# Kernel optimization log

Hardware: AMD Instinct MI355X
Metric: run time of the kernel (lower is better)

The kernel has to match this reference:

```python
import jax, jax.numpy as jnp
import numpy as np

EMBED_DIM = 1024
NUM_HEADS = 16
HEAD_DIM = EMBED_DIM // NUM_HEADS
B, S = 4, 2048


def setup_inputs() -> dict:
    key = jax.random.key(0)
    ks = jax.random.split(key, 9)
    scale = 1.0 / np.sqrt(EMBED_DIM)
    x = jax.random.normal(ks[0], (B, S, EMBED_DIM), dtype=jnp.float32)
    # nn.Linear weights are [out, in]; we store as [in, out] for x @ W
    Wq = jax.random.uniform(ks[1], (EMBED_DIM, EMBED_DIM), jnp.float32, -scale, scale)
    bq = jax.random.uniform(ks[2], (EMBED_DIM,), jnp.float32, -scale, scale)
    Wk = jax.random.uniform(ks[3], (EMBED_DIM, EMBED_DIM), jnp.float32, -scale, scale)
    bk = jax.random.uniform(ks[4], (EMBED_DIM,), jnp.float32, -scale, scale)
    Wv = jax.random.uniform(ks[5], (EMBED_DIM, EMBED_DIM), jnp.float32, -scale, scale)
    bv = jax.random.uniform(ks[6], (EMBED_DIM,), jnp.float32, -scale, scale)
    Wo = jax.random.uniform(ks[7], (EMBED_DIM, EMBED_DIM), jnp.float32, -scale, scale)
    bo = jax.random.uniform(ks[8], (EMBED_DIM,), jnp.float32, -scale, scale)
    return {"x": x, "Wq": Wq, "bq": bq, "Wk": Wk, "bk": bk,
            "Wv": Wv, "bv": bv, "Wo": Wo, "bo": bo}


def reference(x, Wq, bq, Wk, bk, Wv, bv, Wo, bo):
    Bsz, Slen, E = x.shape
    H, D = NUM_HEADS, HEAD_DIM
    # projections -> [B, H, S, D]
    def split_heads(t):
        return t.reshape(Bsz, Slen, H, D).transpose(0, 2, 1, 3)
    q = split_heads(x @ Wq + bq)
    k = split_heads(x @ Wk + bk)
    v = split_heads(x @ Wv + bv)
    # scores [B, H, S, S]
    scores = jnp.einsum('bhqd,bhkd->bhqk', q, k) / jnp.sqrt(jnp.float32(D))
    attn = jax.nn.softmax(scores, axis=-1)  # dropout p=0.0 -> identity
    out = jnp.einsum('bhqk,bhkd->bhqd', attn, v)  # [B, H, S, D]
    out = out.transpose(0, 2, 1, 3).reshape(Bsz, Slen, E)
    return out @ Wo + bo
```

## Files before the change

### kernel.cpp

```cpp
#include <hip/hip_runtime.h>

typedef __bf16 bf16x8 __attribute__((ext_vector_type(8)));
typedef float floatx4 __attribute__((ext_vector_type(4)));

#define B_   4
#define H_   16
#define S_   2048
#define D_   64
#define E_   1024
#define BS_  8192

#define QSCALE 0.18033688011112042f

__device__ __forceinline__ floatx4 mfma16(bf16x8 a, bf16x8 b, floatx4 c) {
  return __builtin_amdgcn_mfma_f32_16x16x32_bf16(a, b, c, 0, 0, 0);
}

__device__ __forceinline__ unsigned short f2bf(float f) {
  union { float f; unsigned int u; } a;
  a.f = f;
  unsigned int u = a.u;
  return (unsigned short)((u + 0x7fffu + ((u >> 16) & 1u)) >> 16);
}

__device__ __forceinline__ unsigned int pack2bf(float a, float b) {
  union { float f; unsigned int u; } ua, ub;
  ua.f = a; ub.f = b;
  return __builtin_amdgcn_perm(ub.u + 0x8000u, ua.u + 0x8000u, 0x07060302u);
}

__device__ __forceinline__ void async16(const unsigned short* g, unsigned short* l) {
  __builtin_amdgcn_global_load_lds(
      (const __attribute__((address_space(1))) unsigned int*)g,
      (__attribute__((address_space(3))) unsigned int*)l, 16, 0, 0);
}

__global__ __launch_bounds__(256) void transpose4(
    const float* __restrict__ W0, const float* __restrict__ W1,
    const float* __restrict__ W2, const float* __restrict__ W3,
    unsigned short* __restrict__ Wt) {
  __shared__ float tile[32][33];
  const float* src = blockIdx.z == 0 ? W0 : blockIdx.z == 1 ? W1
                   : blockIdx.z == 2 ? W2 : W3;
  unsigned short* dst = Wt + (size_t)blockIdx.z * E_ * E_;
  const int k0 = blockIdx.x * 32, n0 = blockIdx.y * 32;
  const int tx = threadIdx.x, ty = threadIdx.y;
#pragma unroll
  for (int i = 0; i < 32; i += 8)
    tile[ty + i][tx] = src[(size_t)(k0 + ty + i) * E_ + n0 + tx];
  __syncthreads();
#pragma unroll
  for (int i = 0; i < 32; i += 8)
    dst[(size_t)(n0 + ty + i) * E_ + k0 + tx] = f2bf(tile[tx][ty + i]);
}

__global__ __launch_bounds__(256) void cast_x(
    const float* __restrict__ x, unsigned short* __restrict__ xb) {
  const size_t i = ((size_t)blockIdx.x * 256 + threadIdx.x) * 8;
  const float4* p = (const float4*)(x + i);
  float4 a0 = p[0], a1 = p[1];
  union { unsigned short h[8]; uint4 u; } pk;
  pk.h[0] = f2bf(a0.x); pk.h[1] = f2bf(a0.y); pk.h[2] = f2bf(a0.z); pk.h[3] = f2bf(a0.w);
  pk.h[4] = f2bf(a1.x); pk.h[5] = f2bf(a1.y); pk.h[6] = f2bf(a1.z); pk.h[7] = f2bf(a1.w);
  *(uint4*)(xb + i) = pk.u;
}

#define GEMM_CORE(APTR, BPTR)                                                  \
  __shared__ __align__(16) unsigned short As[128][32];                         \
  __shared__ __align__(16) unsigned short Bs[128][32];                         \
  const int t = threadIdx.x;                                                   \
  const int w = t >> 6, lane = t & 63, quad = lane >> 4, l15 = lane & 15;      \
  const int moff = (w >> 1) * 64, noff = (w & 1) * 64;                         \
  const int m0 = blockIdx.y * 128, n0 = blockIdx.x * 128;                      \
  const int r_loc = lane >> 2, cphys = lane & 3;                               \
  const int r0 = w * 32 + r_loc, r1 = r0 + 16;                                 \
  const int sw = (r0 & 3) ^ ((r0 >> 2) & 1);         \
  const int clog = (cphys ^ sw) * 8;                                           \
  const unsigned short* gA0 = (APTR) + (size_t)(m0 + r0) * E_ + clog;          \
  const unsigned short* gA1 = (APTR) + (size_t)(m0 + r1) * E_ + clog;          \
  const unsigned short* gB0 = (BPTR) + (size_t)(n0 + r0) * E_ + clog;          \
  const unsigned short* gB1 = (BPTR) + (size_t)(n0 + r1) * E_ + clog;          \
  unsigned short* lA0 = &As[w * 32][0];                                        \
  unsigned short* lA1 = &As[w * 32 + 16][0];                                   \
  unsigned short* lB0 = &Bs[w * 32][0];                                        \
  unsigned short* lB1 = &Bs[w * 32 + 16][0];                                   \
  const int sF = (l15 & 3) ^ ((l15 >> 2) & 1);          \
  const int fcol = ((quad ^ sF)) * 8;                                          \
  floatx4 acc[4][4] = {};                                                      \
  for (int k0 = 0; k0 < E_; k0 += 32) {                                        \
    async16(gA0 + k0, lA0);                                                    \
    async16(gA1 + k0, lA1);                                                    \
    async16(gB0 + k0, lB0);                                                    \
    async16(gB1 + k0, lB1);                                                    \
    __syncthreads();                     \
    bf16x8 af[4], bf[4];                                                       \
    _Pragma("unroll")                                                          \
    for (int i = 0; i < 4; i++)                                                \
      af[i] = *(const bf16x8*)&As[moff + i * 16 + l15][fcol];                  \
    _Pragma("unroll")                                                          \
    for (int j = 0; j < 4; j++)                                                \
      bf[j] = *(const bf16x8*)&Bs[noff + j * 16 + l15][fcol];                  \
    _Pragma("unroll")                                                          \
    for (int i = 0; i < 4; i++)                                                \
      _Pragma("unroll")                                                        \
      for (int j = 0; j < 4; j++) acc[i][j] = mfma16(af[i], bf[j], acc[i][j]); \
    __syncthreads();                              \
  }

__global__ __launch_bounds__(256) void gemm_qkv(
    const unsigned short* __restrict__ xb, const unsigned short* __restrict__ Wt,
    const float* __restrict__ bq, const float* __restrict__ bk,
    const float* __restrict__ bv,
    unsigned short* __restrict__ Q, unsigned short* __restrict__ K,
    unsigned short* __restrict__ V) {
  GEMM_CORE(xb, Wt)

  const int which = n0 >> 10;
  const float* bias = which == 0 ? bq : (which == 1 ? bk : bv);
  unsigned short* dst = which == 0 ? Q : (which == 1 ? K : V);
  const float sc = which == 0 ? QSCALE : 1.0f;
#pragma unroll
  for (int j = 0; j < 4; j++) {
    const int n = (n0 + noff + j * 16 + l15) & 1023;
    const int h = n >> 6, d = n & 63;
    const float bb = bias[n];
#pragma unroll
    for (int i = 0; i < 4; i++) {
#pragma unroll
      for (int r = 0; r < 4; r++) {
        const int m = m0 + moff + i * 16 + quad * 4 + r;
        const int b = m >> 11, s = m & 2047;
        const float val = (acc[i][j][r] + bb) * sc;
        if (which == 2) {
          const int sp = (s & ~63) | (((s & 15) << 2) | ((s >> 4) & 3));
          dst[(((size_t)(b * H_ + h) * D_) + d) * S_ + sp] = f2bf(val);
        } else {
          dst[(((size_t)(b * H_ + h) * S_) + s) * D_ + d] = f2bf(val);
        }
      }
    }
  }
}

__global__ __launch_bounds__(256, 4) void attn_kernel(
    const unsigned short* __restrict__ Q, const unsigned short* __restrict__ K,
    const unsigned short* __restrict__ Vt, unsigned short* __restrict__ AO) {
  __shared__ __align__(16) unsigned short Ks[64][72];
  __shared__ __align__(16) unsigned short Vs[64][72];
  __shared__ __align__(16) unsigned short Ps[128][72];
  const int t = threadIdx.x;
  const int w = t >> 6, lane = t & 63, quad = lane >> 4, l15 = lane & 15;
  const int bh = blockIdx.y;
  const int q0 = blockIdx.x * 128;
  const int qb = w * 32;
  const size_t base = (size_t)bh * S_ * D_;

  bf16x8 qf[2][2];
#pragma unroll
  for (int mt = 0; mt < 2; mt++)
#pragma unroll
    for (int ks = 0; ks < 2; ks++)
      qf[mt][ks] = *(const bf16x8*)(Q + base +
                    (size_t)(q0 + qb + mt * 16 + l15) * D_ + ks * 32 + quad * 8);

  float l_i[2][4] = {};
  floatx4 O[2][4] = {};

  const int kk = t >> 2, cc = (t & 3) * 16;
  const unsigned short* kp = K  + base + (size_t)kk * D_ + cc;
  const unsigned short* vp = Vt + base + (size_t)kk * S_ + cc;

  uint4 kr0 = *(const uint4*)(kp);
  uint4 kr1 = *(const uint4*)(kp + 8);
  uint4 vr0 = *(const uint4*)(vp);
  uint4 vr1 = *(const uint4*)(vp + 8);

  for (int kt0 = 0; kt0 < S_; kt0 += 64) {
    *(uint4*)&Ks[kk][cc]     = kr0;
    *(uint4*)&Ks[kk][cc + 8] = kr1;
    *(uint4*)&Vs[kk][cc]     = vr0;
    *(uint4*)&Vs[kk][cc + 8] = vr1;
    __syncthreads();

    if (kt0 + 64 < S_) {
      kr0 = *(const uint4*)(kp + (size_t)(kt0 + 64) * D_);
      kr1 = *(const uint4*)(kp + (size_t)(kt0 + 64) * D_ + 8);
      vr0 = *(const uint4*)(vp + kt0 + 64);
      vr1 = *(const uint4*)(vp + kt0 + 72);
    }

    floatx4 s[2][4] = {};
#pragma unroll
    for (int kt = 0; kt < 4; kt++) {
#pragma unroll
      for (int ks = 0; ks < 2; ks++) {
        bf16x8 kf = *(const bf16x8*)&Ks[kt * 16 + l15][ks * 32 + quad * 8];
#pragma unroll
        for (int mt = 0; mt < 2; mt++) s[mt][kt] = mfma16(qf[mt][ks], kf, s[mt][kt]);
      }
    }

#pragma unroll
    for (int mt = 0; mt < 2; mt++) {
#pragma unroll
      for (int r = 0; r < 4; r++) {
        const float p0 = __builtin_amdgcn_exp2f(s[mt][0][r]);
        const float p1 = __builtin_amdgcn_exp2f(s[mt][1][r]);
        const float p2 = __builtin_amdgcn_exp2f(s[mt][2][r]);
        const float p3 = __builtin_amdgcn_exp2f(s[mt][3][r]);
        l_i[mt][r] += (p0 + p1) + (p2 + p3);
        uint2 pk;
        pk.x = pack2bf(p0, p1);
        pk.y = pack2bf(p2, p3);
        *(uint2*)((char*)&Ps[qb + mt * 16 + quad * 4 + r][0] + l15 * 8) = pk;
      }
    }

#pragma unroll
    for (int ks = 0; ks < 2; ks++) {
      bf16x8 pf[2];
#pragma unroll
      for (int mt = 0; mt < 2; mt++)
        pf[mt] = *(const bf16x8*)&Ps[qb + mt * 16 + l15][ks * 32 + quad * 8];
#pragma unroll
      for (int dt = 0; dt < 4; dt++) {
        bf16x8 vf = *(const bf16x8*)&Vs[dt * 16 + l15][ks * 32 + quad * 8];
#pragma unroll
        for (int mt = 0; mt < 2; mt++) O[mt][dt] = mfma16(pf[mt], vf, O[mt][dt]);
      }
    }
    __syncthreads();
  }

  const int b = bh >> 4, h = bh & 15;
#pragma unroll
  for (int mt = 0; mt < 2; mt++)
#pragma unroll
    for (int r = 0; r < 4; r++) {
      float sum = l_i[mt][r];
#pragma unroll
      for (int off = 1; off < 16; off <<= 1) sum += __shfl_xor(sum, off, 64);
      const float inv = 1.f / sum;
      const int srow = q0 + qb + mt * 16 + quad * 4 + r;
      unsigned short* aop = AO + (size_t)(b * S_ + srow) * E_ + h * D_ + l15;
#pragma unroll
      for (int dt = 0; dt < 4; dt++)
        aop[dt * 16] = f2bf(O[mt][dt][r] * inv);
    }
}

__global__ __launch_bounds__(256) void gemm_out(
    const unsigned short* __restrict__ A, const unsigned short* __restrict__ Wt,
    const float* __restrict__ bo, float* __restrict__ Cout) {
  GEMM_CORE(A, Wt)

#pragma unroll
  for (int j = 0; j < 4; j++) {
    const int n = n0 + noff + j * 16 + l15;
    const float bb = bo[n];
#pragma unroll
    for (int i = 0; i < 4; i++) {
#pragma unroll
      for (int r = 0; r < 4; r++) {
        const int m = m0 + moff + i * 16 + quad * 4 + r;
        Cout[(size_t)m * E_ + n] = acc[i][j][r] + bb;
      }
    }
  }
}

extern "C" void kernel_launch(void* const* d_in, const int* in_sizes, int n_in,
                              void* d_out, int out_size, void* d_ws, size_t ws_size,
                              hipStream_t stream) {
  const float* x  = (const float*)d_in[0];
  const float* Wq = (const float*)d_in[1];
  const float* bq = (const float*)d_in[2];
  const float* Wk = (const float*)d_in[3];
  const float* bk = (const float*)d_in[4];
  const float* Wv = (const float*)d_in[5];
  const float* bv = (const float*)d_in[6];
  const float* Wo = (const float*)d_in[7];
  const float* bo = (const float*)d_in[8];
  float* out = (float*)d_out;

  unsigned short* Wt = (unsigned short*)d_ws;
  unsigned short* Qb = Wt + (size_t)4 * E_ * E_;
  unsigned short* Kb = Qb + (size_t)B_ * H_ * S_ * D_;
  unsigned short* Vb = Kb + (size_t)B_ * H_ * S_ * D_;
  unsigned short* xb = Vb + (size_t)B_ * H_ * S_ * D_;
  unsigned short* AO = xb;

  transpose4<<<dim3(32, 32, 4), dim3(32, 8), 0, stream>>>(Wq, Wk, Wv, Wo, Wt);
  cast_x<<<dim3(BS_ * E_ / (256 * 8)), 256, 0, stream>>>(x, xb);
  gemm_qkv<<<dim3(24, 64), 256, 0, stream>>>(xb, Wt, bq, bk, bv, Qb, Kb, Vb);
  attn_kernel<<<dim3(16, 64), 256, 0, stream>>>(Qb, Kb, Vb, AO);
  gemm_out<<<dim3(8, 64), 256, 0, stream>>>(AO, Wt + (size_t)3 * E_ * E_, bo, out);
}
```

Before: 318.7 us.

## Triple-buffer GEMM LDS tiles and prefetch next K-slice during MFMA compute

The shared GEMM core now keeps three LDS buffers for the A and B tiles. Before computing on the current slice, it issues the async global-to-LDS loads for the next K slice, which cuts the loop to one barrier per iteration instead of two. The aim is to hide global load latency behind the MFMA work. The cost is three times the LDS footprint (about 48KB per block), which may lower occupancy, and correctness relies on the barrier waiting for the outstanding async loads.

```diff
diff --git a/kernel.cpp b/kernel.cpp
--- a/kernel.cpp
+++ b/kernel.cpp
@@ -66,8 +66,8 @@
 }
 
 #define GEMM_CORE(APTR, BPTR)                                                  \
-  __shared__ __align__(16) unsigned short As[128][32];                         \
-  __shared__ __align__(16) unsigned short Bs[128][32];                         \
+  __shared__ __align__(16) unsigned short As[3][128][32];                      \
+  __shared__ __align__(16) unsigned short Bs[3][128][32];                      \
   const int t = threadIdx.x;                                                   \
   const int w = t >> 6, lane = t & 63, quad = lane >> 4, l15 = lane & 15;      \
   const int moff = (w >> 1) * 64, noff = (w & 1) * 64;                         \
@@ -80,31 +80,37 @@
   const unsigned short* gA1 = (APTR) + (size_t)(m0 + r1) * E_ + clog;          \
   const unsigned short* gB0 = (BPTR) + (size_t)(n0 + r0) * E_ + clog;          \
   const unsigned short* gB1 = (BPTR) + (size_t)(n0 + r1) * E_ + clog;          \
-  unsigned short* lA0 = &As[w * 32][0];                                        \
-  unsigned short* lA1 = &As[w * 32 + 16][0];                                   \
-  unsigned short* lB0 = &Bs[w * 32][0];                                        \
-  unsigned short* lB1 = &Bs[w * 32 + 16][0];                                   \
   const int sF = (l15 & 3) ^ ((l15 >> 2) & 1);          \
   const int fcol = ((quad ^ sF)) * 8;                                          \
   floatx4 acc[4][4] = {};                                                      \
-  for (int k0 = 0; k0 < E_; k0 += 32) {                                        \
-    async16(gA0 + k0, lA0);                                                    \
-    async16(gA1 + k0, lA1);                                                    \
-    async16(gB0 + k0, lB0);                                                    \
-    async16(gB1 + k0, lB1);                                                    \
-    __syncthreads();                     \
+                                                \
+  async16(gA0, &As[0][w * 32][0]);                                             \
+  async16(gA1, &As[0][w * 32 + 16][0]);                                        \
+  async16(gB0, &Bs[0][w * 32][0]);                                             \
+  async16(gB1, &Bs[0][w * 32 + 16][0]);                                        \
+  int cb = 0;                                                                  \
+  for (int it = 0; it < 32; ++it) {                                            \
+    __syncthreads();          \
+    const int nb = cb == 2 ? 0 : cb + 1;                                       \
+    if (it + 1 < 32) {                                                         \
+      const int kn = (it + 1) * 32;                                            \
+      async16(gA0 + kn, &As[nb][w * 32][0]);                                   \
+      async16(gA1 + kn, &As[nb][w * 32 + 16][0]);                              \
+      async16(gB0 + kn, &Bs[nb][w * 32][0]);                                   \
+      async16(gB1 + kn, &Bs[nb][w * 32 + 16][0]);                              \
+    }                                                                          \
     bf16x8 af[4], bf[4];                                                       \
     _Pragma("unroll")                                                          \
     for (int i = 0; i < 4; i++)                                                \
-      af[i] = *(const bf16x8*)&As[moff + i * 16 + l15][fcol];                  \
+      af[i] = *(const bf16x8*)&As[cb][moff + i * 16 + l15][fcol];              \
     _Pragma("unroll")                                                          \
     for (int j = 0; j < 4; j++)                                                \
-      bf[j] = *(const bf16x8*)&Bs[noff + j * 16 + l15][fcol];                  \
+      bf[j] = *(const bf16x8*)&Bs[cb][noff + j * 16 + l15][fcol];              \
     _Pragma("unroll")                                                          \
     for (int i = 0; i < 4; i++)                                                \
       _Pragma("unroll")                                                        \
       for (int j = 0; j < 4; j++) acc[i][j] = mfma16(af[i], bf[j], acc[i][j]); \
-    __syncthreads();                              \
+    cb = nb;                                                                   \
   }
 
 __global__ __launch_bounds__(256) void gemm_qkv(
```

New measurement: 324.8 us. About the same (+1.9%).

## Triple-buffer GEMM LDS tiles with async prefetch two stages ahead

Applied to the files above, without the earlier changes.

Replaces the single-buffered GEMM main loop, which issued async global-to-LDS loads and then stalled on a barrier every k-step, with a three-stage ring of LDS buffers. Loads for tile k+2 are issued while tile k is consumed, using explicit vmcnt waits and one barrier per step instead of two. This is meant to hide global memory latency behind MFMA work, at the cost of three times the LDS footprint, which may reduce occupancy.

```diff
diff --git a/kernel.cpp b/kernel.cpp
--- a/kernel.cpp
+++ b/kernel.cpp
@@ -65,9 +65,42 @@
   *(uint4*)(xb + i) = pk.u;
 }
 
+#define GFRAG_MFMA(CA, CB)                                                     \
+    bf16x8 af[4], bf[4];                                                       \
+    _Pragma("unroll")                                                          \
+    for (int i = 0; i < 4; i++)                                                \
+      af[i] = *(const bf16x8*)&CA[moff + i * 16 + l15][fcol];                  \
+    _Pragma("unroll")                                                          \
+    for (int j = 0; j < 4; j++)                                                \
+      bf[j] = *(const bf16x8*)&CB[noff + j * 16 + l15][fcol];                  \
+    _Pragma("unroll")                                                          \
+    for (int i = 0; i < 4; i++)                                                \
+      _Pragma("unroll")                                                        \
+      for (int j = 0; j < 4; j++) acc[i][j] = mfma16(af[i], bf[j], acc[i][j]);
+
+#define GISSUE(NA, NB, KT)                                                     \
+    { const int kn = (KT) * 32;                                                \
+      async16(gA0 + kn, &NA[w * 32][0]);                                       \
+      async16(gA1 + kn, &NA[w * 32 + 16][0]);                                  \
+      async16(gB0 + kn, &NB[w * 32][0]);                                       \
+      async16(gB1 + kn, &NB[w * 32 + 16][0]); }
+
+#define GSTEP(CA, CB, NA, NB, KT)                                              \
+    { __builtin_amdgcn_s_waitcnt(0x0F74);       \
+      __builtin_amdgcn_s_barrier();                                            \
+      GISSUE(NA, NB, KT)                                                       \
+      GFRAG_MFMA(CA, CB) }
+
+#define GSTEP_TAIL(CA, CB, VM)                                                 \
+    { __builtin_amdgcn_s_waitcnt(VM);                                          \
+      __builtin_amdgcn_s_barrier();                                            \
+      GFRAG_MFMA(CA, CB) }
+
 #define GEMM_CORE(APTR, BPTR)                                                  \
-  __shared__ __align__(16) unsigned short As[128][32];                         \
-  __shared__ __align__(16) unsigned short Bs[128][32];                         \
+  __shared__ __align__(16) unsigned short As0[128][32], As1[128][32],          \
+      As2[128][32];                                                            \
+  __shared__ __align__(16) unsigned short Bs0[128][32], Bs1[128][32],          \
+      Bs2[128][32];                                                            \
   const int t = threadIdx.x;                                                   \
   const int w = t >> 6, lane = t & 63, quad = lane >> 4, l15 = lane & 15;      \
   const int moff = (w >> 1) * 64, noff = (w & 1) * 64;                         \
@@ -80,32 +113,18 @@
   const unsigned short* gA1 = (APTR) + (size_t)(m0 + r1) * E_ + clog;          \
   const unsigned short* gB0 = (BPTR) + (size_t)(n0 + r0) * E_ + clog;          \
   const unsigned short* gB1 = (BPTR) + (size_t)(n0 + r1) * E_ + clog;          \
-  unsigned short* lA0 = &As[w * 32][0];                                        \
-  unsigned short* lA1 = &As[w * 32 + 16][0];                                   \
-  unsigned short* lB0 = &Bs[w * 32][0];                                        \
-  unsigned short* lB1 = &Bs[w * 32 + 16][0];                                   \
   const int sF = (l15 & 3) ^ ((l15 >> 2) & 1);          \
   const int fcol = ((quad ^ sF)) * 8;                                          \
   floatx4 acc[4][4] = {};                                                      \
-  for (int k0 = 0; k0 < E_; k0 += 32) {                                        \
-    async16(gA0 + k0, lA0);                                                    \
-    async16(gA1 + k0, lA1);                                                    \
-    async16(gB0 + k0, lB0);                                                    \
-    async16(gB1 + k0, lB1);                                                    \
-    __syncthreads();                     \
-    bf16x8 af[4], bf[4];                                                       \
-    _Pragma("unroll")                                                          \
-    for (int i = 0; i < 4; i++)                                                \
-      af[i] = *(const bf16x8*)&As[moff + i * 16 + l15][fcol];                  \
-    _Pragma("unroll")                                                          \
-    for (int j = 0; j < 4; j++)                                                \
-      bf[j] = *(const bf16x8*)&Bs[noff + j * 16 + l15][fcol];                  \
-    _Pragma("unroll")                                                          \
-    for (int i = 0; i < 4; i++)                                                \
-      _Pragma("unroll")                                                        \
-      for (int j = 0; j < 4; j++) acc[i][j] = mfma16(af[i], bf[j], acc[i][j]); \
-    __syncthreads();                              \
-  }
+  GISSUE(As0, Bs0, 0)                                     \
+  GISSUE(As1, Bs1, 1)                                     \
+  for (int k3 = 0; k3 < 30; k3 += 3) {                                         \
+    GSTEP(As0, Bs0, As2, Bs2, k3 + 2)                                          \
+    GSTEP(As1, Bs1, As0, Bs0, k3 + 3)                                          \
+    GSTEP(As2, Bs2, As1, Bs1, k3 + 4)                                          \
+  }                                                                            \
+  GSTEP_TAIL(As0, Bs0, 0x0F74)    \
+  GSTEP_TAIL(As1, Bs1, 0x0F70)
 
 __global__ __launch_bounds__(256) void gemm_qkv(
     const unsigned short* __restrict__ xb, const unsigned short* __restrict__ Wt,
```

Result: faster. 298.7 us (-6.3%).

## Load GEMM fragments directly from global memory with register prefetch and padded pitch

Applied to the files above, without the earlier changes.

Replaces the LDS-staged GEMM mainloop with direct per-wave global loads of bf16 MFMA fragments, double-buffered in registers across k-steps, removing all block barriers. Weights, cast activations and attention output are written with a padded row pitch of 1088 to reduce memory channel aliasing on strided row reads. Occupancy hint of 3 blocks is added to the GEMMs. This trades LDS reuse for more global/L2 traffic and larger register usage.

```diff
diff --git a/kernel.cpp b/kernel.cpp
--- a/kernel.cpp
+++ b/kernel.cpp
@@ -9,6 +9,7 @@
 #define D_   64
 #define E_   1024
 #define BS_  8192
+#define PITCH_ 1088
 
 #define QSCALE 0.18033688011112042f
 
@@ -27,12 +28,6 @@
   union { float f; unsigned int u; } ua, ub;
   ua.f = a; ub.f = b;
   return __builtin_amdgcn_perm(ub.u + 0x8000u, ua.u + 0x8000u, 0x07060302u);
-}
-
-__device__ __forceinline__ void async16(const unsigned short* g, unsigned short* l) {
-  __builtin_amdgcn_global_load_lds(
-      (const __attribute__((address_space(1))) unsigned int*)g,
-      (__attribute__((address_space(3))) unsigned int*)l, 16, 0, 0);
 }
 
 __global__ __launch_bounds__(256) void transpose4(
@@ -42,7 +37,7 @@
   __shared__ float tile[32][33];
   const float* src = blockIdx.z == 0 ? W0 : blockIdx.z == 1 ? W1
                    : blockIdx.z == 2 ? W2 : W3;
-  unsigned short* dst = Wt + (size_t)blockIdx.z * E_ * E_;
+  unsigned short* dst = Wt + (size_t)blockIdx.z * E_ * PITCH_;
   const int k0 = blockIdx.x * 32, n0 = blockIdx.y * 32;
   const int tx = threadIdx.x, ty = threadIdx.y;
 #pragma unroll
@@ -51,63 +46,63 @@
   __syncthreads();
 #pragma unroll
   for (int i = 0; i < 32; i += 8)
-    dst[(size_t)(n0 + ty + i) * E_ + k0 + tx] = f2bf(tile[tx][ty + i]);
+    dst[(size_t)(n0 + ty + i) * PITCH_ + k0 + tx] = f2bf(tile[tx][ty + i]);
 }
 
 __global__ __launch_bounds__(256) void cast_x(
     const float* __restrict__ x, unsigned short* __restrict__ xb) {
-  const size_t i = ((size_t)blockIdx.x * 256 + threadIdx.x) * 8;
-  const float4* p = (const float4*)(x + i);
+  const size_t g = (size_t)blockIdx.x * 256 + threadIdx.x;
+  const size_t row = g >> 7;
+  const int col = (int)(g & 127) * 8;
+  const float4* p = (const float4*)(x + row * E_ + col);
   float4 a0 = p[0], a1 = p[1];
   union { unsigned short h[8]; uint4 u; } pk;
   pk.h[0] = f2bf(a0.x); pk.h[1] = f2bf(a0.y); pk.h[2] = f2bf(a0.z); pk.h[3] = f2bf(a0.w);
   pk.h[4] = f2bf(a1.x); pk.h[5] = f2bf(a1.y); pk.h[6] = f2bf(a1.z); pk.h[7] = f2bf(a1.w);
-  *(uint4*)(xb + i) = pk.u;
+  *(uint4*)(xb + row * PITCH_ + col) = pk.u;
 }
 
 #define GEMM_CORE(APTR, BPTR)                                                  \
-  __shared__ __align__(16) unsigned short As[128][32];                         \
-  __shared__ __align__(16) unsigned short Bs[128][32];                         \
   const int t = threadIdx.x;                                                   \
   const int w = t >> 6, lane = t & 63, quad = lane >> 4, l15 = lane & 15;      \
   const int moff = (w >> 1) * 64, noff = (w & 1) * 64;                         \
   const int m0 = blockIdx.y * 128, n0 = blockIdx.x * 128;                      \
-  const int r_loc = lane >> 2, cphys = lane & 3;                               \
-  const int r0 = w * 32 + r_loc, r1 = r0 + 16;                                 \
-  const int sw = (r0 & 3) ^ ((r0 >> 2) & 1);         \
-  const int clog = (cphys ^ sw) * 8;                                           \
-  const unsigned short* gA0 = (APTR) + (size_t)(m0 + r0) * E_ + clog;          \
-  const unsigned short* gA1 = (APTR) + (size_t)(m0 + r1) * E_ + clog;          \
-  const unsigned short* gB0 = (BPTR) + (size_t)(n0 + r0) * E_ + clog;          \
-  const unsigned short* gB1 = (BPTR) + (size_t)(n0 + r1) * E_ + clog;          \
-  unsigned short* lA0 = &As[w * 32][0];                                        \
-  unsigned short* lA1 = &As[w * 32 + 16][0];                                   \
-  unsigned short* lB0 = &Bs[w * 32][0];                                        \
-  unsigned short* lB1 = &Bs[w * 32 + 16][0];                                   \
-  const int sF = (l15 & 3) ^ ((l15 >> 2) & 1);          \
-  const int fcol = ((quad ^ sF)) * 8;                                          \
+  const unsigned short* pa[4];                                                 \
+  const unsigned short* pb[4];                                                 \
+  _Pragma("unroll")                                                            \
+  for (int i = 0; i < 4; i++)                                                  \
+    pa[i] = (APTR) + (size_t)(m0 + moff + i * 16 + l15) * PITCH_ + quad * 8;   \
+  _Pragma("unroll")                                                            \
+  for (int j = 0; j < 4; j++)                                                  \
+    pb[j] = (BPTR) + (size_t)(n0 + noff + j * 16 + l15) * PITCH_ + quad * 8;   \
   floatx4 acc[4][4] = {};                                                      \
-  for (int k0 = 0; k0 < E_; k0 += 32) {                                        \
-    async16(gA0 + k0, lA0);                                                    \
-    async16(gA1 + k0, lA1);                                                    \
-    async16(gB0 + k0, lB0);                                                    \
-    async16(gB1 + k0, lB1);                                                    \
-    __syncthreads();                     \
-    bf16x8 af[4], bf[4];                                                       \
+  bf16x8 afc[4], bfc[4], afn[4], bfn[4];                                       \
+  _Pragma("unroll")                                                            \
+  for (int i = 0; i < 4; i++) afc[i] = *(const bf16x8*)(pa[i]);                \
+  _Pragma("unroll")                                                            \
+  for (int j = 0; j < 4; j++) bfc[j] = *(const bf16x8*)(pb[j]);                \
+  for (int k0 = 0; k0 < E_; k0 += 64) {                                        \
+    _Pragma("unroll")                                                          \
+    for (int i = 0; i < 4; i++) afn[i] = *(const bf16x8*)(pa[i] + k0 + 32);    \
+    _Pragma("unroll")                                                          \
+    for (int j = 0; j < 4; j++) bfn[j] = *(const bf16x8*)(pb[j] + k0 + 32);    \
     _Pragma("unroll")                                                          \
     for (int i = 0; i < 4; i++)                                                \
-      af[i] = *(const bf16x8*)&As[moff + i * 16 + l15][fcol];                  \
-    _Pragma("unroll")                                                          \
-    for (int j = 0; j < 4; j++)                                                \
-      bf[j] = *(const bf16x8*)&Bs[noff + j * 16 + l15][fcol];                  \
+      _Pragma("unroll")                                                        \
+      for (int j = 0; j < 4; j++) acc[i][j] = mfma16(afc[i], bfc[j], acc[i][j]); \
+    if (k0 + 64 < E_) {                                                        \
+      _Pragma("unroll")                                                        \
+      for (int i = 0; i < 4; i++) afc[i] = *(const bf16x8*)(pa[i] + k0 + 64);  \
+      _Pragma("unroll")                                                        \
+      for (int j = 0; j < 4; j++) bfc[j] = *(const bf16x8*)(pb[j] + k0 + 64);  \
+    }                                                                          \
     _Pragma("unroll")                                                          \
     for (int i = 0; i < 4; i++)                                                \
       _Pragma("unroll")                                                        \
-      for (int j = 0; j < 4; j++) acc[i][j] = mfma16(af[i], bf[j], acc[i][j]); \
-    __syncthreads();                              \
-  }
-
-__global__ __launch_bounds__(256) void gemm_qkv(
+      for (int j = 0; j < 4; j++) acc[i][j] = mfma16(afn[i], bfn[j], acc[i][j]); \
+  }
+
+__global__ __launch_bounds__(256, 3) void gemm_qkv(
     const unsigned short* __restrict__ xb, const unsigned short* __restrict__ Wt,
     const float* __restrict__ bq, const float* __restrict__ bk,
     const float* __restrict__ bv,
@@ -242,14 +237,14 @@
       for (int off = 1; off < 16; off <<= 1) sum += __shfl_xor(sum, off, 64);
       const float inv = 1.f / sum;
       const int srow = q0 + qb + mt * 16 + quad * 4 + r;
-      unsigned short* aop = AO + (size_t)(b * S_ + srow) * E_ + h * D_ + l15;
+      unsigned short* aop = AO + (size_t)(b * S_ + srow) * PITCH_ + h * D_ + l15;
 #pragma unroll
       for (int dt = 0; dt < 4; dt++)
         aop[dt * 16] = f2bf(O[mt][dt][r] * inv);
     }
 }
 
-__global__ __launch_bounds__(256) void gemm_out(
+__global__ __launch_bounds__(256, 3) void gemm_out(
     const unsigned short* __restrict__ A, const unsigned short* __restrict__ Wt,
     const float* __restrict__ bo, float* __restrict__ Cout) {
   GEMM_CORE(A, Wt)
@@ -284,15 +279,15 @@
   float* out = (float*)d_out;
 
   unsigned short* Wt = (unsigned short*)d_ws;
-  unsigned short* Qb = Wt + (size_t)4 * E_ * E_;
+  unsigned short* Qb = Wt + (size_t)4 * E_ * PITCH_;
   unsigned short* Kb = Qb + (size_t)B_ * H_ * S_ * D_;
   unsigned short* Vb = Kb + (size_t)B_ * H_ * S_ * D_;
   unsigned short* xb = Vb + (size_t)B_ * H_ * S_ * D_;
   unsigned short* AO = xb;
 
   transpose4<<<dim3(32, 32, 4), dim3(32, 8), 0, stream>>>(Wq, Wk, Wv, Wo, Wt);
-  cast_x<<<dim3(BS_ * E_ / (256 * 8)), 256, 0, stream>>>(x, xb);
+  cast_x<<<dim3(4096), 256, 0, stream>>>(x, xb);
   gemm_qkv<<<dim3(24, 64), 256, 0, stream>>>(xb, Wt, bq, bk, bv, Qb, Kb, Vb);
   attn_kernel<<<dim3(16, 64), 256, 0, stream>>>(Qb, Kb, Vb, AO);
-  gemm_out<<<dim3(8, 64), 256, 0, stream>>>(AO, Wt + (size_t)3 * E_ * E_, bo, out);
-}
+  gemm_out<<<dim3(8, 64), 256, 0, stream>>>(AO, Wt + (size_t)3 * E_ * PITCH_, bo, out);
+}
```

Result: slower. 476.8 us (+49.6%).
